# Kernel optimization log

Measured on AMD Instinct MI355X. Metric: run time of the kernel, lower is better.

The kernel has to match this reference:

```python
import jax, jax.numpy as jnp
from jax import lax
import numpy as np

D_MODEL = 768
D_STATE = 16
D_CONV = 4
EXPAND = 2
D_INNER = EXPAND * D_MODEL
BATCH = 2
SEQ = 512


def setup_inputs() -> dict:
    key = jax.random.key(0)
    ks = jax.random.split(key, 8)
    s = 0.02
    return {
        "x": jax.random.normal(ks[0], (BATCH, SEQ, D_MODEL), jnp.float32),
        "W_in": jax.random.normal(ks[1], (2 * D_INNER, D_MODEL), jnp.float32) * s,
        "conv_w": jax.random.normal(ks[2], (D_INNER, 1, D_CONV), jnp.float32) * s,
        "conv_b": jnp.zeros((D_INNER,), jnp.float32),
        "W_x": jax.random.normal(ks[3], (D_INNER + 2 * D_STATE, D_INNER), jnp.float32) * s,
        "W_dt": jax.random.normal(ks[4], (D_INNER, D_INNER), jnp.float32) * s,
        "b_dt": jnp.zeros((D_INNER,), jnp.float32),
        "A_log": jnp.log(jax.random.uniform(ks[5], (D_INNER, D_STATE), jnp.float32, 1e-4, 1.0)),
        "Dp": jnp.ones((D_INNER,), jnp.float32),
        "W_out": jax.random.normal(ks[6], (D_MODEL, D_INNER), jnp.float32) * s,
    }


def parallel_scan_log(log_coeffs, log_values):
    """Faithful port of ParallelScan.parallel_scan_log (Blelchh-style up/down sweep
    in log space). Indices are static, so the Python loop over O(log L) levels is
    trace-time only."""
    B, L, D = log_coeffs.shape
    if L <= 4:
        run = log_values[:, 0]
        outs = [run]
        for i in range(1, L):
            run = jnp.logaddexp(run, log_coeffs[:, i] + log_values[:, i])
            outs.append(run)
        return jnp.stack(outs, axis=1)
    levels = int(np.ceil(np.log2(L)))
    coeffs, values = log_coeffs, log_values
    # up-sweep
    for level in range(levels):
        step = 2 ** (level + 1)
        if step - 1 >= L:
            break
        right = np.arange(step - 1, L, step)
        left = right - 2 ** level
        m = (left >= 0) & (right < L)
        left, right = left[m], right[m]
        if left.size == 0:
            continue
        new_c = coeffs[:, left] + coeffs[:, right]
        new_v = jnp.logaddexp(values[:, left], coeffs[:, right] + values[:, right])
        coeffs = coeffs.at[:, right].set(new_c)
        values = values.at[:, right].set(new_v)
    # down-sweep
    for level in range(levels - 1, -1, -1):
        step = 2 ** (level + 1)
        if step - 1 >= L:
            continue
        right = np.arange(step - 1, L, step)
        left = right - 2 ** level
        m = (left >= 0) & (right < L)
        left, right = left[m], right[m]
        if left.size == 0:
            continue
        tmp = values[:, right]
        new_r = jnp.logaddexp(values[:, left], coeffs[:, right] + values[:, right])
        values = values.at[:, right].set(new_r)
        values = values.at[:, left].set(tmp)
    return values


def reference(x, W_in, conv_w, conv_b, W_x, W_dt, b_dt, A_log, Dp, W_out):
    Bsz, L, _ = x.shape
    xz = x @ W_in.T                                 # [B, L, 2*d_inner]
    x_inner, z = jnp.split(xz, 2, axis=-1)
    # depthwise causal conv1d (pad left d_conv-1, truncate to L == torch slice)
    xc = jnp.transpose(x_inner, (0, 2, 1))          # [B, d_inner, L]
    xc = lax.conv_general_dilated(
        xc, conv_w, (1,), [(D_CONV - 1, 0)],
        dimension_numbers=("NCH", "OIH", "NCH"),
        feature_group_count=D_INNER)
    xc = xc + conv_b[None, :, None]
    x_conv = jax.nn.silu(jnp.transpose(xc, (0, 2, 1)))  # [B, L, d_inner]
    x_dbl = x_conv @ W_x.T                              # [B, L, d_inner + 2*d_state]
    delta, Bmat, Cmat = jnp.split(x_dbl, [D_INNER, D_INNER + D_STATE], axis=-1)
    delta = jax.nn.softplus(delta @ W_dt.T + b_dt)      # [B, L, d_inner]
    # selective scan
    A = -jnp.exp(A_log)                                 # [d_inner, d_state]
    deltaA = jnp.exp(jnp.einsum("bld,dn->bldn", delta, A))
    deltaB_u = jnp.einsum("bld,bln,bld->bldn", delta, Bmat, x_conv)
    log_coeffs = jnp.log(deltaA + 1e-12).reshape(Bsz, L, -1)
    log_values = jnp.log(jnp.abs(deltaB_u) + 1e-12).reshape(Bsz, L, -1)
    scanned = jnp.exp(parallel_scan_log(log_coeffs, log_values))
    scanned = scanned.reshape(Bsz, L, D_INNER, D_STATE)
    y = jnp.einsum("bldn,bln->bld", scanned, Cmat) + x_conv * Dp
    y = y * jax.nn.silu(z)
    return y @ W_out.T
```

## Files before the change

kernel.cpp:

```cpp
#include <hip/hip_runtime.h>
#include <math.h>

#define D_MODEL 768
#define D_STATE 16
#define D_CONV  4
#define D_INNER 1536
#define BATCH   2
#define SEQ     512
#define M_ROWS  (BATCH * SEQ)
#define N_XZ    (2 * D_INNER)
#define N_XDBL  (D_INNER + 2 * D_STATE)

typedef _Float16 half8 __attribute__((ext_vector_type(8)));
typedef float  f32x4  __attribute__((ext_vector_type(4)));
typedef unsigned short ushort_t;
typedef ushort_t ushort8_t __attribute__((ext_vector_type(8)));

__device__ __forceinline__ ushort_t f2h(float f) {
    _Float16 h = (_Float16)f;
    return *(ushort_t*)&h;
}
__device__ __forceinline__ void pack8(const float* s, ushort_t* d) {
    ushort8_t o;
#pragma unroll
    for (int j = 0; j < 8; ++j) o[j] = f2h(s[j]);
    *(ushort8_t*)d = o;
}
__device__ __forceinline__ void gld16(const ushort_t* g, void* l) {
    __builtin_amdgcn_global_load_lds((const __attribute__((address_space(1))) void*)g,
                                     (__attribute__((address_space(3))) void*)l, 16, 0, 0);
}

#define SX   (M_ROWS * D_MODEL)
#define SW1  (N_XZ * D_MODEL)
#define SW2  (N_XDBL * D_INNER)
#define SWDT (D_INNER * D_INNER)
#define SWO  (D_MODEL * D_INNER)
#define SPACK (SX + SW1 + SW2 + SWDT + SWO)
__global__ __launch_bounds__(256) void pack_kernel(
    const float* __restrict__ x, const float* __restrict__ win,
    const float* __restrict__ wx, const float* __restrict__ wdt,
    const float* __restrict__ wo,
    ushort_t* __restrict__ xs, ushort_t* __restrict__ w1, ushort_t* __restrict__ w2,
    ushort_t* __restrict__ wdt16, ushort_t* __restrict__ wo16)
{
    long i = ((long)blockIdx.x * 256 + threadIdx.x) * 8;
    if (i >= SPACK) return;
    const float* src; ushort_t* dst; long base;
    if (i < SX)                         { src = x;   dst = xs;    base = i; }
    else if (i < SX + SW1)              { src = win; dst = w1;    base = i - SX; }
    else if (i < SX + SW1 + SW2)        { src = wx;  dst = w2;    base = i - SX - SW1; }
    else if (i < SX + SW1 + SW2 + SWDT) { src = wdt; dst = wdt16; base = i - SX - SW1 - SW2; }
    else                                { src = wo;  dst = wo16;  base = i - SX - SW1 - SW2 - SWDT; }
    float v[8];
    *(float4*)(v)     = *(const float4*)(src + base);
    *(float4*)(v + 4) = *(const float4*)(src + base + 4);
    pack8(v, dst + base);
}

__global__ __launch_bounds__(256) void gemm_lds(
    const ushort_t* __restrict__ A, int lda,
    const ushort_t* __restrict__ B, int ldb,
    float* __restrict__ Cbase, long pstride, int ldc,
    int N, int kc)
{
    __shared__ ushort_t smA[3][4096];
    __shared__ ushort_t smB[3][4096];

    const int tid  = threadIdx.x;
    const int w    = tid >> 6;
    const int lane = tid & 63;
    const int lr   = lane & 15;
    const int lq   = lane >> 4;

    const int Gx = gridDim.x, Gy = gridDim.y;
    const int T = Gx * Gy * gridDim.z;
    const int f = blockIdx.x + Gx * (blockIdx.y + Gy * blockIdx.z);
    const int g = (T & 7) ? f : ((f & 7) * (T >> 3) + (f >> 3));
    const int bx = g % Gx;
    const int by = (g / Gx) % Gy;
    const int z  = g / (Gx * Gy);
    float* __restrict__ C = Cbase + (long)z * pstride;

    const int bm = by * 128;
    const int bn = bx * 128;
    const int k0base = z * kc;

    auto stage = [&](int buf, int k0) {
#pragma unroll
        for (int i = 0; i < 2; ++i) {
            const int gA = i * 4 + w;
            const int rA = bm + gA * 16 + lr;
            gld16(A + (long)rA * lda + k0 + lq * 8, &smA[buf][gA * 512]);
        }
#pragma unroll
        for (int i = 0; i < 2; ++i) {
            const int gB = i * 4 + w;
            int rB = bn + gB * 16 + lr; if (rB >= N) rB = N - 1;
            gld16(B + (long)rB * ldb + k0 + lq * 8, &smB[buf][gB * 512]);
        }
    };

    f32x4 acc[4][4] = {};
    const int wm = (w & 1) * 64;
    const int wn = (w >> 1) * 64;

    stage(0, k0base);
    const int nIter = kc >> 5;
    int cur = 0;
    for (int it = 0; it < nIter; ++it) {
        const int nxt = (cur == 2) ? 0 : cur + 1;
        if (it + 1 < nIter) {
            stage(nxt, k0base + (it + 1) * 32);
            asm volatile("s_waitcnt vmcnt(4)" ::: "memory");
        } else {
            asm volatile("s_waitcnt vmcnt(0)" ::: "memory");
        }
        __builtin_amdgcn_s_barrier();
        asm volatile("" ::: "memory");

        half8 ah[4], bh[4];
#pragma unroll
        for (int mt = 0; mt < 4; ++mt)
            ah[mt] = *(const half8*)&smA[cur][(((w & 1) * 4 + mt) * 512) + lq * 128 + lr * 8];
#pragma unroll
        for (int nt = 0; nt < 4; ++nt)
            bh[nt] = *(const half8*)&smB[cur][(((w >> 1) * 4 + nt) * 512) + lq * 128 + lr * 8];
#pragma unroll
        for (int mt = 0; mt < 4; ++mt)
#pragma unroll
            for (int nt = 0; nt < 4; ++nt)
                acc[mt][nt] = __builtin_amdgcn_mfma_f32_16x16x32_f16(ah[mt], bh[nt], acc[mt][nt], 0, 0, 0);
        cur = nxt;
    }

#pragma unroll
    for (int mt = 0; mt < 4; ++mt)
#pragma unroll
        for (int nt = 0; nt < 4; ++nt)
#pragma unroll
            for (int r = 0; r < 4; ++r) {
                int row = bm + wm + mt * 16 + lq * 4 + r;
                int col = bn + wn + nt * 16 + lr;
                if (col >= N) continue;
                C[(long)row * ldc + col] = acc[mt][nt][r];
            }
}

__global__ __launch_bounds__(256) void conv_silu_kernel(
    const float* __restrict__ p0, const float* __restrict__ p1,
    const float* __restrict__ conv_w, const float* __restrict__ conv_b,
    float* __restrict__ xconvT, float* __restrict__ zsiluT,
    ushort_t* __restrict__ xc)
{
    __shared__ float Tx[64][17];
    __shared__ float Tz[64][17];
    const int rb = blockIdx.x;
    const int db = blockIdx.y;
    const int dl = threadIdx.x & 63;
    const int d  = db * 64 + dl;
    const int rr = threadIdx.x >> 6;
    const float w0 = conv_w[d * 4 + 0], w1 = conv_w[d * 4 + 1];
    const float w2 = conv_w[d * 4 + 2], w3 = conv_w[d * 4 + 3];
    const float bb = conv_b[d];
#pragma unroll
    for (int q = 0; q < 4; ++q) {
        const int r = rb * 16 + q * 4 + rr;
        const int l = r & (SEQ - 1);
        float acc = bb;
        if (l >= 3) { long o = (long)(r - 3) * N_XZ + d; acc = fmaf(w0, p0[o] + p1[o], acc); }
        if (l >= 2) { long o = (long)(r - 2) * N_XZ + d; acc = fmaf(w1, p0[o] + p1[o], acc); }
        if (l >= 1) { long o = (long)(r - 1) * N_XZ + d; acc = fmaf(w2, p0[o] + p1[o], acc); }
        { long o = (long)r * N_XZ + d; acc = fmaf(w3, p0[o] + p1[o], acc); }
        float s = acc / (1.f + expf(-acc));
        xc[(long)r * D_INNER + d] = f2h(s);
        long oz = (long)r * N_XZ + D_INNER + d;
        float zv = p0[oz] + p1[oz];
        Tx[dl][q * 4 + rr] = s;
        Tz[dl][q * 4 + rr] = zv / (1.f + expf(-zv));
    }
    __syncthreads();
    const int rp = threadIdx.x & 15;
    const int dp = threadIdx.x >> 4;
#pragma unroll
    for (int p = 0; p < 4; ++p) {
        int dd = p * 16 + dp;
        long o = (long)(db * 64 + dd) * M_ROWS + rb * 16 + rp;
        xconvT[o] = Tx[dd][rp];
        zsiluT[o] = Tz[dd][rp];
    }
}

__global__ __launch_bounds__(256) void ep_xdbl_kernel(
    const float* __restrict__ P, long ps,
    ushort_t* __restrict__ xd, float* __restrict__ BCT)
{
    long i = ((long)blockIdx.x * 256 + threadIdx.x) * 8;
    if (i >= (long)M_ROWS * N_XDBL) return;
    int row = (int)(i / N_XDBL);
    int col = (int)(i - (long)row * N_XDBL);
    float f[8];
#pragma unroll
    for (int j = 0; j < 8; ++j) f[j] = P[i + j] + P[i + j + ps] + P[i + j + 2 * ps];
    pack8(f, xd + i);
    if (col >= D_INNER) {
#pragma unroll
        for (int j = 0; j < 8; ++j)
            BCT[(long)(col + j - D_INNER) * M_ROWS + row] = f[j];
    }
}

__global__ __launch_bounds__(256) void ep_merge_kernel(
    const float* __restrict__ P, long ps, float* __restrict__ out)
{
    long i = ((long)blockIdx.x * 256 + threadIdx.x) * 8;
    if (i >= (long)M_ROWS * D_MODEL) return;
    float o[8];
#pragma unroll
    for (int j = 0; j < 8; ++j) {
        float v = 0.f;
#pragma unroll
        for (int z = 0; z < 6; ++z) v += P[i + j + z * ps];
        o[j] = v;
    }
    *(float4*)(out + i)     = *(float4*)(o);
    *(float4*)(out + i + 4) = *(float4*)(o + 4);
}

__global__ __launch_bounds__(256) void scan_kernel(
    const float* __restrict__ P, long ps,
    const float* __restrict__ b_dt,
    const float* __restrict__ xconvT,
    const float* __restrict__ zsiluT,
    const float* __restrict__ BCT,
    const float* __restrict__ A_log,
    const float* __restrict__ Dp,
    float* __restrict__ uT)
{
    __shared__ float dlT[512];
    __shared__ float xrT[512];
    __shared__ float red[3 * 512];

    const int bid = blockIdx.x;
    const int b   = bid / D_INNER;
    const int d   = bid % D_INNER;
    const int tid = threadIdx.x;
    const int w   = tid >> 6;
    const int t   = tid & 63;
    const long od = (long)d * M_ROWS + b * SEQ;

    const float bdt = b_dt[d];
#pragma unroll
    for (int q = 0; q < 2; ++q) {
        const int l = tid + q * 256;
        float v = P[od + l] + P[od + l + ps] + P[od + l + 2 * ps] + P[od + l + 3 * ps] + bdt;
        float sp = fmaxf(v, 0.f) + log1pf(expf(-fabsf(v)));
        const int li = (l & 7) * 64 + (l >> 3);
        dlT[li] = sp;
        xrT[li] = xconvT[od + l];
    }
    __syncthreads();

    float dl[8], xr[8], dx[8], yac[8];
#pragma unroll
    for (int j = 0; j < 8; ++j) {
        dl[j] = dlT[j * 64 + t];
        xr[j] = xrT[j * 64 + t];
        dx[j] = dl[j] * xr[j];
        yac[j] = 0.f;
    }
    const int l0 = 8 * t;

#pragma unroll
    for (int nn = 0; nn < 4; ++nn) {
        const int n = w * 4 + nn;
        const float Adn = -expf(A_log[d * D_STATE + n]);
        const float4* Bp = (const float4*)(BCT + (long)n * M_ROWS + b * SEQ + l0);
        float4 b0 = Bp[0], b1 = Bp[1];
        float Bv[8] = {b0.x, b0.y, b0.z, b0.w, b1.x, b1.y, b1.z, b1.w};
        float c[8], v[8];
#pragma unroll
        for (int j = 0; j < 8; ++j) {
            c[j] = __expf(dl[j] * Adn);
            v[j] = fabsf(dx[j] * Bv[j]);
        }
        float c01 = c[1] * c[0], v01 = fmaf(c[1], v[0], v[1]);
        float c23 = c[3] * c[2], v23 = fmaf(c[3], v[2], v[3]);
        float c45 = c[5] * c[4], v45 = fmaf(c[5], v[4], v[5]);
        float c67 = c[7] * c[6], v67 = fmaf(c[7], v[6], v[7]);
        float c03 = c23 * c01,  v03 = fmaf(c23, v01, v23);
        float c47 = c67 * c45,  v47 = fmaf(c67, v45, v67);
        float cA  = c47 * c03,  vA  = fmaf(c47, v03, v47);
#pragma unroll
        for (int h = 1; h <= 32; h <<= 1) {
            float cl = __shfl_up(cA, (unsigned)h);
            float vl = __shfl_up(vA, (unsigned)h);
            if (t >= h) { vA = fmaf(cA, vl, vA); cA = cA * cl; }
        }
        float s = __shfl_up(vA, 1u);
        if (t == 0) s = 0.f;
        const float4* Cp = (const float4*)(BCT + (long)(16 + n) * M_ROWS + b * SEQ + l0);
        float4 c0 = Cp[0], c1 = Cp[1];
        float Cv[8] = {c0.x, c0.y, c0.z, c0.w, c1.x, c1.y, c1.z, c1.w};
#pragma unroll
        for (int j = 0; j < 8; ++j) {
            s = fmaf(c[j], s, v[j]);
            yac[j] = fmaf(s, Cv[j], yac[j]);
        }
    }

    if (w) {
#pragma unroll
        for (int j = 0; j < 8; ++j) red[(w - 1) * 512 + j * 64 + t] = yac[j];
    }
    __syncthreads();
    if (w == 0) {
        const float Dpd = Dp[d];
#pragma unroll
        for (int j = 0; j < 8; ++j) {
            float y = yac[j] + red[j * 64 + t] + red[512 + j * 64 + t] + red[1024 + j * 64 + t];
            float uv = fmaf(xr[j], Dpd, y) * zsiluT[od + l0 + j];
            uT[od + l0 + j] = uv;
        }
    }
}

__global__ __launch_bounds__(256) void transpose_split_kernel(
    const float* __restrict__ uT, ushort_t* __restrict__ u)
{
    __shared__ float T[64][65];
    const int m0 = blockIdx.x * 64;
    const int d0 = blockIdx.y * 64;
    const int c  = threadIdx.x & 63;
    const int rr = threadIdx.x >> 6;
#pragma unroll
    for (int p = 0; p < 64; p += 4)
        T[p + rr][c] = uT[(long)(d0 + p + rr) * M_ROWS + m0 + c];
    __syncthreads();
#pragma unroll
    for (int p = 0; p < 64; p += 4) {
        int rm = p + rr;
        float v = T[c][rm];
        u[(long)(m0 + rm) * D_INNER + (d0 + c)] = f2h(v);
    }
}

extern "C" void kernel_launch(void* const* d_in, const int* in_sizes, int n_in,
                              void* d_out, int out_size, void* d_ws, size_t ws_size,
                              hipStream_t stream)
{
    (void)in_sizes; (void)n_in; (void)out_size; (void)ws_size;

    const float* x      = (const float*)d_in[0];
    const float* W_in   = (const float*)d_in[1];
    const float* conv_w = (const float*)d_in[2];
    const float* conv_b = (const float*)d_in[3];
    const float* W_x    = (const float*)d_in[4];
    const float* W_dt   = (const float*)d_in[5];
    const float* b_dt   = (const float*)d_in[6];
    const float* A_log  = (const float*)d_in[7];
    const float* Dp     = (const float*)d_in[8];
    const float* W_out  = (const float*)d_in[9];
    float* out = (float*)d_out;

    float* ws = (float*)d_ws;
    long off = 0;
    float* P      = ws + off; off += 2L * M_ROWS * N_XZ;
    float* xconvT = ws + off; off += (long)D_INNER * M_ROWS;
    float* zsiluT = ws + off; off += (long)D_INNER * M_ROWS;
    float* uT     = ws + off; off += (long)D_INNER * M_ROWS;
    float* xsbuf  = ws + off; off += (long)M_ROWS * D_MODEL / 2;
    float* w1buf  = ws + off; off += (long)N_XZ * D_MODEL / 2;
    float* w2buf  = ws + off; off += (long)N_XDBL * D_INNER / 2;
    float* wdtbuf = ws + off; off += (long)D_INNER * D_INNER / 2;
    float* wobuf  = ws + off; off += (long)D_MODEL * D_INNER / 2;
    float* xcbuf  = ws + off; off += (long)M_ROWS * D_INNER / 2;
    float* xdbuf  = ws + off; off += (long)M_ROWS * N_XDBL / 2;
    float* BCT    = ws + off; off += (long)2 * D_STATE * M_ROWS;

    ushort_t* xs    = (ushort_t*)xsbuf;
    ushort_t* w1    = (ushort_t*)w1buf;
    ushort_t* w2    = (ushort_t*)w2buf;
    ushort_t* wdt16 = (ushort_t*)wdtbuf;
    ushort_t* wo16  = (ushort_t*)wobuf;
    ushort_t* xc    = (ushort_t*)xcbuf;
    ushort_t* xd    = (ushort_t*)xdbuf;
    ushort_t* u_i   = (ushort_t*)xcbuf;
    float* P6       = P;

    const long psG4 = (long)D_INNER * M_ROWS;

    dim3 blk(256);

    pack_kernel<<<dim3(SPACK / 2048), blk, 0, stream>>>(
        x, W_in, W_x, W_dt, W_out, xs, w1, w2, wdt16, wo16);
    gemm_lds<<<dim3(N_XZ / 128, M_ROWS / 128, 2), blk, 0, stream>>>(
        xs, D_MODEL, w1, D_MODEL, P, (long)M_ROWS * N_XZ, N_XZ, N_XZ, D_MODEL / 2);
    conv_silu_kernel<<<dim3(M_ROWS / 16, D_INNER / 64), blk, 0, stream>>>(
        P, P + (long)M_ROWS * N_XZ, conv_w, conv_b, xconvT, zsiluT, xc);
    gemm_lds<<<dim3((N_XDBL + 127) / 128, M_ROWS / 128, 3), blk, 0, stream>>>(
        xc, D_INNER, w2, D_INNER, P, (long)M_ROWS * N_XDBL, N_XDBL, N_XDBL, D_INNER / 3);
    ep_xdbl_kernel<<<dim3((M_ROWS * N_XDBL) / 2048), blk, 0, stream>>>(
        P, (long)M_ROWS * N_XDBL, xd, BCT);
    gemm_lds<<<dim3(M_ROWS / 128, D_INNER / 128, 4), blk, 0, stream>>>(
        wdt16, D_INNER, xd, N_XDBL, P, psG4, M_ROWS, M_ROWS, D_INNER / 4);
    scan_kernel<<<dim3(BATCH * D_INNER), blk, 0, stream>>>(
        P, psG4, b_dt, xconvT, zsiluT, BCT, A_log, Dp, uT);
    transpose_split_kernel<<<dim3(M_ROWS / 64, D_INNER / 64), blk, 0, stream>>>(
        uT, u_i);
    gemm_lds<<<dim3(D_MODEL / 128, M_ROWS / 128, 6), blk, 0, stream>>>(
        u_i, D_INNER, wo16, D_INNER, P6, (long)M_ROWS * D_MODEL, D_MODEL, D_MODEL, D_INNER / 6);
    ep_merge_kernel<<<dim3((M_ROWS * D_MODEL) / 2048), blk, 0, stream>>>(
        P6, (long)M_ROWS * D_MODEL, out);
}
```

Baseline: 206.3 us.

## Use BK=64 double-buffered GEMM stages and raise split-K factors

The GEMM's LDS pipeline changes from three 32-wide K stages to two 64-wide K stages. The next stage is now issued right after a full vmcnt(0) wait and barrier, so there are fewer barriers per unit of K but less prefetch depth. Because K per split must now be a multiple of 64, the x_dbl GEMM moves from split-K 3 to 4 and the output GEMM from 6 to 8. The epilogues sum the extra partials, and the workspace is reordered so the larger partial buffer fits. More partial-sum traffic and the loss of the third in-flight stage may offset the gains from fewer barriers and more blocks.

```diff
diff --git a/kernel.cpp b/kernel.cpp
--- a/kernel.cpp
+++ b/kernel.cpp
@@ -64,8 +64,8 @@
     float* __restrict__ Cbase, long pstride, int ldc,
     int N, int kc)
 {
-    __shared__ ushort_t smA[3][4096];
-    __shared__ ushort_t smB[3][4096];
+    __shared__ ushort_t smA[2][8192];
+    __shared__ ushort_t smB[2][8192];
 
     const int tid  = threadIdx.x;
     const int w    = tid >> 6;
@@ -88,16 +88,18 @@
 
     auto stage = [&](int buf, int k0) {
 #pragma unroll
-        for (int i = 0; i < 2; ++i) {
-            const int gA = i * 4 + w;
+        for (int i = 0; i < 4; ++i) {
+            const int gh = i * 4 + w;
+            const int gA = gh >> 1, h = gh & 1;
             const int rA = bm + gA * 16 + lr;
-            gld16(A + (long)rA * lda + k0 + lq * 8, &smA[buf][gA * 512]);
-        }
-#pragma unroll
-        for (int i = 0; i < 2; ++i) {
-            const int gB = i * 4 + w;
+            gld16(A + (long)rA * lda + k0 + h * 32 + lq * 8, &smA[buf][gh * 512]);
+        }
+#pragma unroll
+        for (int i = 0; i < 4; ++i) {
+            const int gh = i * 4 + w;
+            const int gB = gh >> 1, h = gh & 1;
             int rB = bn + gB * 16 + lr; if (rB >= N) rB = N - 1;
-            gld16(B + (long)rB * ldb + k0 + lq * 8, &smB[buf][gB * 512]);
+            gld16(B + (long)rB * ldb + k0 + h * 32 + lq * 8, &smB[buf][gh * 512]);
         }
     };
 
@@ -105,33 +107,31 @@
     const int wm = (w & 1) * 64;
     const int wn = (w >> 1) * 64;
 
+    const int nIter = kc >> 6;
     stage(0, k0base);
-    const int nIter = kc >> 5;
     int cur = 0;
     for (int it = 0; it < nIter; ++it) {
-        const int nxt = (cur == 2) ? 0 : cur + 1;
-        if (it + 1 < nIter) {
-            stage(nxt, k0base + (it + 1) * 32);
-            asm volatile("s_waitcnt vmcnt(4)" ::: "memory");
-        } else {
-            asm volatile("s_waitcnt vmcnt(0)" ::: "memory");
-        }
+        asm volatile("s_waitcnt vmcnt(0)" ::: "memory");
         __builtin_amdgcn_s_barrier();
         asm volatile("" ::: "memory");
-
-        half8 ah[4], bh[4];
-#pragma unroll
-        for (int mt = 0; mt < 4; ++mt)
-            ah[mt] = *(const half8*)&smA[cur][(((w & 1) * 4 + mt) * 512) + lq * 128 + lr * 8];
-#pragma unroll
-        for (int nt = 0; nt < 4; ++nt)
-            bh[nt] = *(const half8*)&smB[cur][(((w >> 1) * 4 + nt) * 512) + lq * 128 + lr * 8];
-#pragma unroll
-        for (int mt = 0; mt < 4; ++mt)
+        if (it + 1 < nIter) stage(cur ^ 1, k0base + (it + 1) * 64);
+
+#pragma unroll
+        for (int s = 0; s < 2; ++s) {
+            half8 ah[4], bh[4];
+#pragma unroll
+            for (int mt = 0; mt < 4; ++mt)
+                ah[mt] = *(const half8*)&smA[cur][((((w & 1) * 4 + mt) * 2 + s) * 512) + lq * 128 + lr * 8];
 #pragma unroll
             for (int nt = 0; nt < 4; ++nt)
-                acc[mt][nt] = __builtin_amdgcn_mfma_f32_16x16x32_f16(ah[mt], bh[nt], acc[mt][nt], 0, 0, 0);
-        cur = nxt;
+                bh[nt] = *(const half8*)&smB[cur][((((w >> 1) * 4 + nt) * 2 + s) * 512) + lq * 128 + lr * 8];
+#pragma unroll
+            for (int mt = 0; mt < 4; ++mt)
+#pragma unroll
+                for (int nt = 0; nt < 4; ++nt)
+                    acc[mt][nt] = __builtin_amdgcn_mfma_f32_16x16x32_f16(ah[mt], bh[nt], acc[mt][nt], 0, 0, 0);
+        }
+        cur ^= 1;
     }
 
 #pragma unroll
@@ -201,7 +201,8 @@
     int col = (int)(i - (long)row * N_XDBL);
     float f[8];
 #pragma unroll
-    for (int j = 0; j < 8; ++j) f[j] = P[i + j] + P[i + j + ps] + P[i + j + 2 * ps];
+    for (int j = 0; j < 8; ++j)
+        f[j] = P[i + j] + P[i + j + ps] + P[i + j + 2 * ps] + P[i + j + 3 * ps];
     pack8(f, xd + i);
     if (col >= D_INNER) {
 #pragma unroll
@@ -220,7 +221,7 @@
     for (int j = 0; j < 8; ++j) {
         float v = 0.f;
 #pragma unroll
-        for (int z = 0; z < 6; ++z) v += P[i + j + z * ps];
+        for (int z = 0; z < 8; ++z) v += P[i + j + z * ps];
         o[j] = v;
     }
     *(float4*)(out + i)     = *(float4*)(o);
@@ -366,9 +367,9 @@
     float* ws = (float*)d_ws;
     long off = 0;
     float* P      = ws + off; off += 2L * M_ROWS * N_XZ;
+    float* uT     = ws + off; off += (long)M_ROWS * N_XDBL;
     float* xconvT = ws + off; off += (long)D_INNER * M_ROWS;
     float* zsiluT = ws + off; off += (long)D_INNER * M_ROWS;
-    float* uT     = ws + off; off += (long)D_INNER * M_ROWS;
     float* xsbuf  = ws + off; off += (long)M_ROWS * D_MODEL / 2;
     float* w1buf  = ws + off; off += (long)N_XZ * D_MODEL / 2;
     float* w2buf  = ws + off; off += (long)N_XDBL * D_INNER / 2;
@@ -388,6 +389,7 @@
     ushort_t* u_i   = (ushort_t*)xcbuf;
     float* P6       = P;
 
+    const long psG3 = (long)M_ROWS * N_XDBL;
     const long psG4 = (long)D_INNER * M_ROWS;
 
     dim3 blk(256);
@@ -398,18 +400,18 @@
         xs, D_MODEL, w1, D_MODEL, P, (long)M_ROWS * N_XZ, N_XZ, N_XZ, D_MODEL / 2);
     conv_silu_kernel<<<dim3(M_ROWS / 16, D_INNER / 64), blk, 0, stream>>>(
         P, P + (long)M_ROWS * N_XZ, conv_w, conv_b, xconvT, zsiluT, xc);
-    gemm_lds<<<dim3((N_XDBL + 127) / 128, M_ROWS / 128, 3), blk, 0, stream>>>(
-        xc, D_INNER, w2, D_INNER, P, (long)M_ROWS * N_XDBL, N_XDBL, N_XDBL, D_INNER / 3);
+    gemm_lds<<<dim3((N_XDBL + 127) / 128, M_ROWS / 128, 4), blk, 0, stream>>>(
+        xc, D_INNER, w2, D_INNER, P, psG3, N_XDBL, N_XDBL, D_INNER / 4);
     ep_xdbl_kernel<<<dim3((M_ROWS * N_XDBL) / 2048), blk, 0, stream>>>(
-        P, (long)M_ROWS * N_XDBL, xd, BCT);
+        P, psG3, xd, BCT);
     gemm_lds<<<dim3(M_ROWS / 128, D_INNER / 128, 4), blk, 0, stream>>>(
         wdt16, D_INNER, xd, N_XDBL, P, psG4, M_ROWS, M_ROWS, D_INNER / 4);
     scan_kernel<<<dim3(BATCH * D_INNER), blk, 0, stream>>>(
         P, psG4, b_dt, xconvT, zsiluT, BCT, A_log, Dp, uT);
     transpose_split_kernel<<<dim3(M_ROWS / 64, D_INNER / 64), blk, 0, stream>>>(
         uT, u_i);
-    gemm_lds<<<dim3(D_MODEL / 128, M_ROWS / 128, 6), blk, 0, stream>>>(
-        u_i, D_INNER, wo16, D_INNER, P6, (long)M_ROWS * D_MODEL, D_MODEL, D_MODEL, D_INNER / 6);
+    gemm_lds<<<dim3(D_MODEL / 128, M_ROWS / 128, 8), blk, 0, stream>>>(
+        u_i, D_INNER, wo16, D_INNER, P6, (long)M_ROWS * D_MODEL, D_MODEL, D_MODEL, D_INNER / 8);
     ep_merge_kernel<<<dim3((M_ROWS * D_MODEL) / 2048), blk, 0, stream>>>(
         P6, (long)M_ROWS * D_MODEL, out);
 }
```

After: 210.3 us. Within noise of the previous version (+1.9%).
